# Kernel tuning notes

Measured on AMD Instinct MI355X. Metric: run time of the kernel, lower is better.

Reference implementation:

```python
import jax, jax.numpy as jnp
import numpy as np

B, T, C = 2, 2048, 1024
H, HD = 16, 64
M = 256  # per memory bank
K_CANON = 4


def setup_inputs() -> dict:
    key = jax.random.key(0)
    ks = jax.random.split(key, 10)
    s = 0.02
    return {
        "x": jax.random.normal(ks[0], (B, T, C), jnp.float32),
        "fwd_mem": jax.random.normal(ks[1], (B, M, C), jnp.float32),
        "rev_mem": jax.random.normal(ks[2], (B, M, C), jnp.float32),
        "Wq": jax.random.normal(ks[3], (C, C), jnp.float32) * s,
        "Wk": jax.random.normal(ks[4], (C, C), jnp.float32) * s,
        "Wv": jax.random.normal(ks[5], (C, C), jnp.float32) * s,
        "Wo": jax.random.normal(ks[6], (C, C), jnp.float32) * s,
        "gate_w": jax.random.normal(ks[7], (H, C), jnp.float32) * s,
        "gate_b": jnp.zeros((H,), jnp.float32),
        "canon_w": jax.random.normal(ks[8], (C, 1, K_CANON), jnp.float32) * s,
        "canon_bias": jax.random.normal(ks[9], (C,), jnp.float32) * s,
    }


def _canon_conv(y, canon_w, canon_bias):
    # causal depthwise conv1d with residual; torch weight [C,1,K] -> WIO kernel [K,1,C]
    kern = jnp.transpose(canon_w, (2, 1, 0))
    y_pad = jnp.pad(y, ((0, 0), (K_CANON - 1, 0), (0, 0)))
    conv = jax.lax.conv_general_dilated(
        y_pad, kern, window_strides=(1,), padding='VALID',
        dimension_numbers=('NWC', 'WIO', 'NWC'), feature_group_count=C)
    return y + conv + canon_bias


def reference(x, fwd_mem, rev_mem, Wq, Wk, Wv, Wo, gate_w, gate_b, canon_w, canon_bias):
    Bn, Tn, Cn = x.shape
    scale = 1.0 / np.sqrt(HD)

    q = x @ Wq.T  # [B,T,C]
    k = x @ Wk.T
    v = x @ Wv.T
    # memory integration: project memories with same k/v proj, concat on seq dim
    k = jnp.concatenate([k, fwd_mem @ Wk.T, rev_mem @ Wk.T], axis=1)  # [B,S,C]
    v = jnp.concatenate([v, fwd_mem @ Wv.T, rev_mem @ Wv.T], axis=1)
    S = k.shape[1]
    mem_len = S - Tn

    def heads(t):
        return t.reshape(Bn, -1, H, HD).transpose(0, 2, 1, 3)  # [B,h,S,hd]

    qh, kh, vh = heads(q), heads(k), heads(v)
    scores = jnp.einsum('bhtd,bhsd->bhts', qh, kh) * scale  # [B,h,T,S]
    # causal mask over the first T key columns; memory columns fully visible
    causal = jnp.triu(jnp.ones((Tn, Tn), bool), k=1)
    full_mask = jnp.pad(causal, ((0, 0), (0, mem_len)))  # [T,S]
    scores = jnp.where(full_mask[None, None], -jnp.inf, scores)
    w = jax.nn.softmax(scores, axis=-1)

    # split chunk vs memory, gate memory contribution per head
    w_chunk, w_mem = w[..., :Tn], w[..., Tn:]
    v_chunk, v_mem = vh[:, :, :Tn], vh[:, :, Tn:]
    Y_chunk = jnp.einsum('bhts,bhsd->bhtd', w_chunk, v_chunk)
    Y_mem = jnp.einsum('bhtm,bhmd->bhtd', w_mem, v_mem)
    g = jax.nn.sigmoid(q @ gate_w.T + gate_b)  # [B,T,h]
    g = g.transpose(0, 2, 1)[..., None]  # [B,h,T,1]
    Y = Y_chunk + g * Y_mem

    attn_out = Y.transpose(0, 2, 1, 3).reshape(Bn, Tn, Cn)
    attn_out = _canon_conv(attn_out, canon_w, canon_bias)
    return attn_out @ Wo.T
```

## Files before the change

kernel.cpp:

```cpp
#include <hip/hip_runtime.h>
#include <hip/hip_bf16.h>
#include <cstdint>


typedef __bf16 bf16x8_t __attribute__((ext_vector_type(8)));
typedef __bf16 bf16x4_t __attribute__((ext_vector_type(4)));
typedef float f32x4_t __attribute__((ext_vector_type(4)));

__device__ __forceinline__ f32x4_t mfma16(bf16x8_t a, bf16x8_t b, f32x4_t c) {
    return __builtin_amdgcn_mfma_f32_16x16x32_bf16(a, b, c, 0, 0, 0);
}

__device__ __forceinline__ void gl2lds16(const void* g, void* l) {
    __builtin_amdgcn_global_load_lds(
        (__attribute__((address_space(1))) uint32_t*)(uintptr_t)g,
        (__attribute__((address_space(3))) uint32_t*)l, 16, 0, 0);
}

#define OFF_X   0
#define OFF_FWD 4194304
#define OFF_REV 4718592
#define OFF_WQ  5242880
#define OFF_WK  6291456
#define OFF_WV  7340032
#define OFF_WO  8388608
#define OFF_GW  9437184
#define OFF_GB  9453568
#define OFF_CW  9453584
#define OFF_CB  9457680
#define N_TOT   9458704

__global__ __launch_bounds__(256) void conv_all_kernel(
    const void* p0, const void* p1, const void* p2, const void* p3,
    const void* p4, const void* p5, const void* p6, const void* p7,
    const void* p8, const void* p9, const void* p10,
    __hip_bfloat16* __restrict__ arena)
{
    const int i = (blockIdx.x * 256 + threadIdx.x) * 4;
    if (i >= N_TOT) return;
    const void* src; int off;
    if      (i < OFF_FWD) { src = p0;  off = OFF_X;   }
    else if (i < OFF_REV) { src = p1;  off = OFF_FWD; }
    else if (i < OFF_WQ)  { src = p2;  off = OFF_REV; }
    else if (i < OFF_WK)  { src = p3;  off = OFF_WQ;  }
    else if (i < OFF_WV)  { src = p4;  off = OFF_WK;  }
    else if (i < OFF_WO)  { src = p5;  off = OFF_WV;  }
    else if (i < OFF_GW)  { src = p6;  off = OFF_WO;  }
    else if (i < OFF_GB)  { src = p7;  off = OFF_GW;  }
    else if (i < OFF_CW)  { src = p8;  off = OFF_GB;  }
    else if (i < OFF_CB)  { src = p9;  off = OFF_CW;  }
    else                  { src = p10; off = OFF_CB;  }
    const int j = i - off;
    const float4 f = *(const float4*)((const float*)src + j);
    arena[i + 0] = __float2bfloat16(f.x);
    arena[i + 1] = __float2bfloat16(f.y);
    arena[i + 2] = __float2bfloat16(f.z);
    arena[i + 3] = __float2bfloat16(f.w);
}

__device__ __forceinline__ void gemm_core(
    const __hip_bfloat16* __restrict__ A, const __hip_bfloat16* __restrict__ B,
    void* __restrict__ C, int ldc, int f32o, int arow0, int brow0,
    __hip_bfloat16* As, __hip_bfloat16* Bs)
{
    const int tid  = threadIdx.x;
    const int lane = tid & 63;
    const int wid  = tid >> 6;
    const int q4   = lane >> 4;
    const int c16  = lane & 15;
    const int wm   = (wid >> 1) * 64;
    const int wn   = (wid & 1) * 64;
    const int c0 = tid;
    const int c1 = tid + 256;
    const __hip_bfloat16* gA0 = A + (size_t)(arow0 + (c0 >> 2)) * 1024 + ((c0 & 3) << 3);
    const __hip_bfloat16* gA1 = A + (size_t)(arow0 + (c1 >> 2)) * 1024 + ((c1 & 3) << 3);
    const __hip_bfloat16* gB0 = B + (size_t)(brow0 + (c0 >> 2)) * 1024 + ((c0 & 3) << 3);
    const __hip_bfloat16* gB1 = B + (size_t)(brow0 + (c1 >> 2)) * 1024 + ((c1 & 3) << 3);

    f32x4_t acc[4][4];
#pragma unroll
    for (int i = 0; i < 4; ++i)
#pragma unroll
        for (int j = 0; j < 4; ++j)
#pragma unroll
            for (int r = 0; r < 4; ++r) acc[i][j][r] = 0.0f;

    gl2lds16(gA0, As + c0 * 8);
    gl2lds16(gA1, As + c1 * 8);
    gl2lds16(gB0, Bs + c0 * 8);
    gl2lds16(gB1, Bs + c1 * 8);

    for (int it = 0; it < 32; ++it) {
        __hip_bfloat16* curA = As + (it & 1) * 4096;
        __hip_bfloat16* curB = Bs + (it & 1) * 4096;
        __syncthreads();
        if (it < 31) {
            const int nk = (it + 1) * 32;
            __hip_bfloat16* nA = As + ((it + 1) & 1) * 4096;
            __hip_bfloat16* nB = Bs + ((it + 1) & 1) * 4096;
            gl2lds16(gA0 + nk, nA + c0 * 8);
            gl2lds16(gA1 + nk, nA + c1 * 8);
            gl2lds16(gB0 + nk, nB + c0 * 8);
            gl2lds16(gB1 + nk, nB + c1 * 8);
        }
        bf16x8_t af[4], bfr[4];
#pragma unroll
        for (int i = 0; i < 4; ++i)
            af[i] = *(const bf16x8_t*)&curA[(wm + i * 16 + c16) * 32 + q4 * 8];
#pragma unroll
        for (int j = 0; j < 4; ++j)
            bfr[j] = *(const bf16x8_t*)&curB[(wn + j * 16 + c16) * 32 + q4 * 8];
#pragma unroll
        for (int i = 0; i < 4; ++i)
#pragma unroll
            for (int j = 0; j < 4; ++j)
                acc[i][j] = mfma16(af[i], bfr[j], acc[i][j]);
    }
#pragma unroll
    for (int i = 0; i < 4; ++i) {
        const int mg = arow0 + wm + i * 16 + q4 * 4;
#pragma unroll
        for (int j = 0; j < 4; ++j) {
            const int ng = brow0 + wn + j * 16 + c16;
#pragma unroll
            for (int r = 0; r < 4; ++r) {
                const size_t idx = (size_t)(mg + r) * ldc + ng;
                if (f32o) ((float*)C)[idx] = acc[i][j][r];
                else ((__hip_bfloat16*)C)[idx] = __float2bfloat16(acc[i][j][r]);
            }
        }
    }
}

__global__ __launch_bounds__(256) void qkv_kernel(
    const __hip_bfloat16* __restrict__ x, const __hip_bfloat16* __restrict__ Wqk,
    const __hip_bfloat16* __restrict__ Wv,
    __hip_bfloat16* __restrict__ QK, __hip_bfloat16* __restrict__ Vt)
{
    __shared__ __align__(16) __hip_bfloat16 As[2 * 128 * 32];
    __shared__ __align__(16) __hip_bfloat16 Bs[2 * 128 * 32];
    int id = blockIdx.x;
    if (id < 640)
        gemm_core(x, Wqk, QK, 2048, 0, (id >> 4) * 128, (id & 15) * 128, As, Bs);
    else {
        id -= 640;
        gemm_core(Wv, x, Vt, 5120, 0, (id & 7) * 128, (id >> 3) * 128, As, Bs);
    }
}

__global__ __launch_bounds__(256) void gemm_bt_kernel(
    const __hip_bfloat16* __restrict__ A, const __hip_bfloat16* __restrict__ B,
    void* __restrict__ C, int ldc, int f32o)
{
    __shared__ __align__(16) __hip_bfloat16 As[2 * 128 * 32];
    __shared__ __align__(16) __hip_bfloat16 Bs[2 * 128 * 32];
    gemm_core(A, B, C, ldc, f32o, blockIdx.x * 128, blockIdx.y * 128, As, Bs);
}

__global__ __launch_bounds__(64) void gate_kernel(
    const __hip_bfloat16* __restrict__ QK, const __hip_bfloat16* __restrict__ gw,
    const __hip_bfloat16* __restrict__ gb, float* __restrict__ G)
{
    const int base = blockIdx.x * 16;
    const int lane = threadIdx.x;
    const int q4   = lane >> 4;
    const int c16  = lane & 15;
    f32x4_t acc = {0.0f, 0.0f, 0.0f, 0.0f};
    const __hip_bfloat16* qrow = QK + (size_t)(base + c16) * 2048 + q4 * 8;
    const __hip_bfloat16* wrow = gw + (size_t)c16 * 1024 + q4 * 8;
#pragma unroll
    for (int kk = 0; kk < 32; ++kk) {
        const bf16x8_t a = *(const bf16x8_t*)(qrow + kk * 32);
        const bf16x8_t w = *(const bf16x8_t*)(wrow + kk * 32);
        acc = mfma16(a, w, acc);
    }
    const float bias = __bfloat162float(gb[c16]);
#pragma unroll
    for (int r = 0; r < 4; ++r) {
        const int row = base + q4 * 4 + r;
        G[(size_t)row * 16 + c16] = 1.0f / (1.0f + __expf(-(acc[r] + bias)));
    }
}

#define PSTR 72
__global__ __launch_bounds__(256) void attn_kernel(
    const __hip_bfloat16* __restrict__ QK,
    const __hip_bfloat16* __restrict__ Vt,
    const float* __restrict__ G, __hip_bfloat16* __restrict__ Y)
{
    __shared__ __align__(16) __hip_bfloat16 Ks[64 * 64];
    __shared__ __align__(16) __hip_bfloat16 Vs[64 * 64];
    __shared__ __align__(16) __hip_bfloat16 Plds[4][16 * PSTR];
    const int flat = blockIdx.x;
    const int bh   = flat & 31;
    const int tIdx = 31 - (flat >> 5);
    const int b    = bh >> 4;
    const int h    = bh & 15;
    const int tid  = threadIdx.x;
    const int wid  = tid >> 6;
    const int lane = tid & 63;
    const int q4   = lane >> 4;
    const int c16  = lane & 15;
    const int rowbase = tIdx * 64 + wid * 16;

    const __hip_bfloat16* qrow = QK + (size_t)(b * 2048 + rowbase + c16) * 2048 + h * 64;
    const bf16x8_t qa0 = *(const bf16x8_t*)(qrow + q4 * 8);
    const bf16x8_t qa1 = *(const bf16x8_t*)(qrow + 32 + q4 * 8);

    float rs[4], gate[4];
    f32x4_t acc[4];
#pragma unroll
    for (int fp = 0; fp < 4; ++fp)
#pragma unroll
        for (int r = 0; r < 4; ++r) acc[fp][r] = 0.0f;
#pragma unroll
    for (int r = 0; r < 4; ++r) {
        rs[r] = 0.0f;
        gate[r] = G[(size_t)(b * 2048 + rowbase + q4 * 4 + r) * 16 + h];
    }

    const int nCausal = tIdx + 1;
    const int nTiles  = nCausal + 8;
    auto kvRow = [&](int tile) -> int {
        if (tile < nCausal) return b * 2048 + tile * 64;
        const int mi = (tile - nCausal) * 64;
        return (mi < 256) ? 4096 + b * 256 + mi : 4608 + b * 256 + (mi - 256);
    };

    const int srow0 = tid >> 3,         sch0 = (tid & 7) ^ (srow0 & 7);
    const int srow1 = (tid + 256) >> 3, sch1 = (tid & 7) ^ (srow1 & 7);
    const int sw0 = (q4 ^ (c16 & 7)) * 8;
    const int sw1 = ((q4 + 4) ^ (c16 & 7)) * 8;
    const __hip_bfloat16* Kbase = QK + 1024 + h * 64;

    for (int tile = 0; tile < nTiles; ++tile) {
        const bool isMem  = (tile >= nCausal);
        const bool isDiag = (tile == nCausal - 1);
        const int  vr     = kvRow(tile);
        __syncthreads();
        gl2lds16(Kbase + (size_t)(vr + srow0) * 2048 + sch0 * 8, &Ks[tid * 8]);
        gl2lds16(Kbase + (size_t)(vr + srow1) * 2048 + sch1 * 8, &Ks[(tid + 256) * 8]);
        gl2lds16(Vt + (size_t)(h * 64 + srow0) * 5120 + vr + sch0 * 8, &Vs[tid * 8]);
        gl2lds16(Vt + (size_t)(h * 64 + srow1) * 5120 + vr + sch1 * 8, &Vs[(tid + 256) * 8]);
        __syncthreads();
        bf16x8_t kb0[4], kb1[4], vb0[4], vb1[4];
#pragma unroll
        for (int f = 0; f < 4; ++f) {
            kb0[f] = *(const bf16x8_t*)&Ks[(f * 16 + c16) * 64 + sw0];
            kb1[f] = *(const bf16x8_t*)&Ks[(f * 16 + c16) * 64 + sw1];
            vb0[f] = *(const bf16x8_t*)&Vs[(f * 16 + c16) * 64 + sw0];
            vb1[f] = *(const bf16x8_t*)&Vs[(f * 16 + c16) * 64 + sw1];
        }
        f32x4_t sc[4];
#pragma unroll
        for (int f = 0; f < 4; ++f) {
            f32x4_t z = {0.0f, 0.0f, 0.0f, 0.0f};
            z = mfma16(qa0, kb0[f], z);
            z = mfma16(qa1, kb1[f], z);
            sc[f] = z;
        }
#pragma unroll
        for (int f = 0; f < 4; ++f)
#pragma unroll
            for (int r = 0; r < 4; ++r) {
                float p = __expf(sc[f][r] * 0.125f);
                if (isDiag) {
                    const int sg = tile * 64 + f * 16 + c16;
                    if (sg > rowbase + q4 * 4 + r) p = 0.0f;
                }
                rs[r] += p;
                if (isMem) p *= gate[r];
                Plds[wid][(q4 * 4 + r) * PSTR + f * 16 + c16] = __float2bfloat16(p);
            }
        const bf16x8_t pa0 = *(const bf16x8_t*)&Plds[wid][c16 * PSTR + q4 * 8];
        const bf16x8_t pa1 = *(const bf16x8_t*)&Plds[wid][c16 * PSTR + 32 + q4 * 8];
#pragma unroll
        for (int fp = 0; fp < 4; ++fp) {
            acc[fp] = mfma16(pa0, vb0[fp], acc[fp]);
            acc[fp] = mfma16(pa1, vb1[fp], acc[fp]);
        }
    }
#pragma unroll
    for (int m = 1; m <= 8; m <<= 1)
#pragma unroll
        for (int r = 0; r < 4; ++r) rs[r] += __shfl_xor(rs[r], m, 64);
    float inv[4];
#pragma unroll
    for (int r = 0; r < 4; ++r) inv[r] = 1.0f / rs[r];
#pragma unroll
    for (int fp = 0; fp < 4; ++fp)
#pragma unroll
        for (int r = 0; r < 4; ++r) {
            const int tg = rowbase + q4 * 4 + r;
            Y[(size_t)(b * 2048 + tg) * 1024 + h * 64 + fp * 16 + c16] =
                __float2bfloat16(acc[fp][r] * inv[r]);
        }
}

__global__ __launch_bounds__(256) void canon_kernel(
    const __hip_bfloat16* __restrict__ Yin, const __hip_bfloat16* __restrict__ cw,
    const __hip_bfloat16* __restrict__ cb, __hip_bfloat16* __restrict__ Yout)
{
    const int idx = (blockIdx.x * 256 + threadIdx.x) * 4;
    const int c = idx & 1023;
    const int t = (idx >> 10) & 2047;
    const bf16x4_t y0 = *(const bf16x4_t*)(Yin + idx);
    const bf16x4_t bb = *(const bf16x4_t*)(cb + c);
    float a[4];
#pragma unroll
    for (int i = 0; i < 4; ++i) a[i] = (float)y0[i] + (float)bb[i];
    const bf16x8_t w01 = *(const bf16x8_t*)(cw + c * 4);
    const bf16x8_t w23 = *(const bf16x8_t*)(cw + c * 4 + 8);
#pragma unroll
    for (int j = 0; j < 4; ++j) {
        if (t - 3 + j >= 0) {
            const bf16x4_t yj = *(const bf16x4_t*)(Yin + idx + (j - 3) * 1024);
            a[0] += (float)yj[0] * (float)w01[j];
            a[1] += (float)yj[1] * (float)w01[4 + j];
            a[2] += (float)yj[2] * (float)w23[j];
            a[3] += (float)yj[3] * (float)w23[4 + j];
        }
    }
    bf16x4_t o;
#pragma unroll
    for (int i = 0; i < 4; ++i) o[i] = (__bf16)a[i];
    *(bf16x4_t*)(Yout + idx) = o;
}

extern "C" void kernel_launch(void* const* d_in, const int* in_sizes, int n_in,
                              void* d_out, int out_size, void* d_ws, size_t ws_size,
                              hipStream_t stream)
{
    char* ws = (char*)d_ws;
    const size_t MB = 1ull << 20;
    if (ws_size < 50 * MB) return;

    __hip_bfloat16* arena = (__hip_bfloat16*)ws;
    __hip_bfloat16* QK    = (__hip_bfloat16*)(ws + 19 * MB);
    __hip_bfloat16* Vt    = (__hip_bfloat16*)(ws + 39 * MB);
    float*          G     = (float*)(ws + 49 * MB);
    __hip_bfloat16* Y1    = (__hip_bfloat16*)ws;
    __hip_bfloat16* Y2    = QK;

    const dim3 blk(256);
    conv_all_kernel<<<dim3((N_TOT / 4 + 255) / 256), blk, 0, stream>>>(
        d_in[0], d_in[1], d_in[2], d_in[3], d_in[4], d_in[5], d_in[6],
        d_in[7], d_in[8], d_in[9], d_in[10], arena);

    const __hip_bfloat16* xB  = arena + OFF_X;
    const __hip_bfloat16* WqB = arena + OFF_WQ;
    const __hip_bfloat16* WvB = arena + OFF_WV;
    const __hip_bfloat16* WoB = arena + OFF_WO;

    qkv_kernel<<<dim3(960), blk, 0, stream>>>(xB, WqB, WvB, QK, Vt);
    gate_kernel<<<dim3(256), dim3(64), 0, stream>>>(QK, arena + OFF_GW, arena + OFF_GB, G);
    attn_kernel<<<dim3(1024), blk, 0, stream>>>(QK, Vt, G, Y1);
    canon_kernel<<<dim3(4096), blk, 0, stream>>>(Y1, arena + OFF_CW, arena + OFF_CB, Y2);
    gemm_bt_kernel<<<dim3(32, 8), blk, 0, stream>>>(Y2, WoB, d_out, 1024, 1);
}
```

Baseline: 241.2 us.

## Double-buffer K/V tiles in attention and compute row sums with MFMA

The attention kernel now keeps two LDS buffers for K and V. It prefetches the next tile while computing the current one, which removes one barrier per tile and hides global load latency behind MFMA work. Row sums of the probabilities come from an MFMA against a ones vector instead of scalar adds and shuffles. Chunk and memory contributions go into separate accumulators, and the gate is applied once in the epilogue rather than per element. The softmax uses exp2 with the log2(e) factor folded into the scale. The costs are doubled K/V LDS usage, which may lower occupancy, extra accumulator registers, and row sums now taken from bf16-rounded probabilities.

After: 248.7 us. 3.1% more time.

```diff
diff --git a/kernel.cpp b/kernel.cpp
--- a/kernel.cpp
+++ b/kernel.cpp
@@ -188,8 +188,8 @@
     const __hip_bfloat16* __restrict__ Vt,
     const float* __restrict__ G, __hip_bfloat16* __restrict__ Y)
 {
-    __shared__ __align__(16) __hip_bfloat16 Ks[64 * 64];
-    __shared__ __align__(16) __hip_bfloat16 Vs[64 * 64];
+    __shared__ __align__(16) __hip_bfloat16 Ks[2][64 * 64];
+    __shared__ __align__(16) __hip_bfloat16 Vs[2][64 * 64];
     __shared__ __align__(16) __hip_bfloat16 Plds[4][16 * PSTR];
     const int flat = blockIdx.x;
     const int bh   = flat & 31;
@@ -207,17 +207,17 @@
     const bf16x8_t qa0 = *(const bf16x8_t*)(qrow + q4 * 8);
     const bf16x8_t qa1 = *(const bf16x8_t*)(qrow + 32 + q4 * 8);
 
-    float rs[4], gate[4];
-    f32x4_t acc[4];
+    bf16x8_t ones;
+#pragma unroll
+    for (int i = 0; i < 8; ++i) ones[i] = (__bf16)1.0f;
+
+    f32x4_t accC[4], accM[4];
+    f32x4_t rsC = {0.0f, 0.0f, 0.0f, 0.0f};
+    f32x4_t rsM = {0.0f, 0.0f, 0.0f, 0.0f};
 #pragma unroll
     for (int fp = 0; fp < 4; ++fp)
 #pragma unroll
-        for (int r = 0; r < 4; ++r) acc[fp][r] = 0.0f;
-#pragma unroll
-    for (int r = 0; r < 4; ++r) {
-        rs[r] = 0.0f;
-        gate[r] = G[(size_t)(b * 2048 + rowbase + q4 * 4 + r) * 16 + h];
-    }
+        for (int r = 0; r < 4; ++r) { accC[fp][r] = 0.0f; accM[fp][r] = 0.0f; }
 
     const int nCausal = tIdx + 1;
     const int nTiles  = nCausal + 8;
@@ -233,23 +233,36 @@
     const int sw1 = ((q4 + 4) ^ (c16 & 7)) * 8;
     const __hip_bfloat16* Kbase = QK + 1024 + h * 64;
 
+    {
+        const int vr0 = kvRow(0);
+        gl2lds16(Kbase + (size_t)(vr0 + srow0) * 2048 + sch0 * 8, &Ks[0][tid * 8]);
+        gl2lds16(Kbase + (size_t)(vr0 + srow1) * 2048 + sch1 * 8, &Ks[0][(tid + 256) * 8]);
+        gl2lds16(Vt + (size_t)(h * 64 + srow0) * 5120 + vr0 + sch0 * 8, &Vs[0][tid * 8]);
+        gl2lds16(Vt + (size_t)(h * 64 + srow1) * 5120 + vr0 + sch1 * 8, &Vs[0][(tid + 256) * 8]);
+    }
+
+    const float SCL = 0.18033688f;
+
     for (int tile = 0; tile < nTiles; ++tile) {
+        const int cur = tile & 1;
+        __syncthreads();
+        if (tile + 1 < nTiles) {
+            const int nxt = cur ^ 1;
+            const int vr  = kvRow(tile + 1);
+            gl2lds16(Kbase + (size_t)(vr + srow0) * 2048 + sch0 * 8, &Ks[nxt][tid * 8]);
+            gl2lds16(Kbase + (size_t)(vr + srow1) * 2048 + sch1 * 8, &Ks[nxt][(tid + 256) * 8]);
+            gl2lds16(Vt + (size_t)(h * 64 + srow0) * 5120 + vr + sch0 * 8, &Vs[nxt][tid * 8]);
+            gl2lds16(Vt + (size_t)(h * 64 + srow1) * 5120 + vr + sch1 * 8, &Vs[nxt][(tid + 256) * 8]);
+        }
         const bool isMem  = (tile >= nCausal);
         const bool isDiag = (tile == nCausal - 1);
-        const int  vr     = kvRow(tile);
-        __syncthreads();
-        gl2lds16(Kbase + (size_t)(vr + srow0) * 2048 + sch0 * 8, &Ks[tid * 8]);
-        gl2lds16(Kbase + (size_t)(vr + srow1) * 2048 + sch1 * 8, &Ks[(tid + 256) * 8]);
-        gl2lds16(Vt + (size_t)(h * 64 + srow0) * 5120 + vr + sch0 * 8, &Vs[tid * 8]);
-        gl2lds16(Vt + (size_t)(h * 64 + srow1) * 5120 + vr + sch1 * 8, &Vs[(tid + 256) * 8]);
-        __syncthreads();
         bf16x8_t kb0[4], kb1[4], vb0[4], vb1[4];
 #pragma unroll
         for (int f = 0; f < 4; ++f) {
-            kb0[f] = *(const bf16x8_t*)&Ks[(f * 16 + c16) * 64 + sw0];
-            kb1[f] = *(const bf16x8_t*)&Ks[(f * 16 + c16) * 64 + sw1];
-            vb0[f] = *(const bf16x8_t*)&Vs[(f * 16 + c16) * 64 + sw0];
-            vb1[f] = *(const bf16x8_t*)&Vs[(f * 16 + c16) * 64 + sw1];
+            kb0[f] = *(const bf16x8_t*)&Ks[cur][(f * 16 + c16) * 64 + sw0];
+            kb1[f] = *(const bf16x8_t*)&Ks[cur][(f * 16 + c16) * 64 + sw1];
+            vb0[f] = *(const bf16x8_t*)&Vs[cur][(f * 16 + c16) * 64 + sw0];
+            vb1[f] = *(const bf16x8_t*)&Vs[cur][(f * 16 + c16) * 64 + sw1];
         }
         f32x4_t sc[4];
 #pragma unroll
@@ -263,37 +276,47 @@
         for (int f = 0; f < 4; ++f)
 #pragma unroll
             for (int r = 0; r < 4; ++r) {
-                float p = __expf(sc[f][r] * 0.125f);
+                float p = __builtin_amdgcn_exp2f(sc[f][r] * SCL);
                 if (isDiag) {
-                    const int sg = tile * 64 + f * 16 + c16;
-                    if (sg > rowbase + q4 * 4 + r) p = 0.0f;
+                    const int sg = f * 16 + c16;
+                    if (sg > wid * 16 + q4 * 4 + r) p = 0.0f;
                 }
-                rs[r] += p;
-                if (isMem) p *= gate[r];
                 Plds[wid][(q4 * 4 + r) * PSTR + f * 16 + c16] = __float2bfloat16(p);
             }
         const bf16x8_t pa0 = *(const bf16x8_t*)&Plds[wid][c16 * PSTR + q4 * 8];
         const bf16x8_t pa1 = *(const bf16x8_t*)&Plds[wid][c16 * PSTR + 32 + q4 * 8];
-#pragma unroll
-        for (int fp = 0; fp < 4; ++fp) {
-            acc[fp] = mfma16(pa0, vb0[fp], acc[fp]);
-            acc[fp] = mfma16(pa1, vb1[fp], acc[fp]);
-        }
-    }
-#pragma unroll
-    for (int m = 1; m <= 8; m <<= 1)
-#pragma unroll
-        for (int r = 0; r < 4; ++r) rs[r] += __shfl_xor(rs[r], m, 64);
-    float inv[4];
-#pragma unroll
-    for (int r = 0; r < 4; ++r) inv[r] = 1.0f / rs[r];
+        if (isMem) {
+            rsM = mfma16(pa0, ones, rsM);
+            rsM = mfma16(pa1, ones, rsM);
+#pragma unroll
+            for (int fp = 0; fp < 4; ++fp) {
+                accM[fp] = mfma16(pa0, vb0[fp], accM[fp]);
+                accM[fp] = mfma16(pa1, vb1[fp], accM[fp]);
+            }
+        } else {
+            rsC = mfma16(pa0, ones, rsC);
+            rsC = mfma16(pa1, ones, rsC);
+#pragma unroll
+            for (int fp = 0; fp < 4; ++fp) {
+                accC[fp] = mfma16(pa0, vb0[fp], accC[fp]);
+                accC[fp] = mfma16(pa1, vb1[fp], accC[fp]);
+            }
+        }
+    }
+
+    float inv[4], gate[4];
+#pragma unroll
+    for (int r = 0; r < 4; ++r) {
+        gate[r] = G[(size_t)(b * 2048 + rowbase + q4 * 4 + r) * 16 + h];
+        inv[r] = 1.0f / (rsC[r] + rsM[r]);
+    }
 #pragma unroll
     for (int fp = 0; fp < 4; ++fp)
 #pragma unroll
         for (int r = 0; r < 4; ++r) {
             const int tg = rowbase + q4 * 4 + r;
             Y[(size_t)(b * 2048 + tg) * 1024 + h * 64 + fp * 16 + c16] =
-                __float2bfloat16(acc[fp][r] * inv[r]);
+                __float2bfloat16((accC[fp][r] + gate[r] * accM[fp][r]) * inv[r]);
         }
 }
 
```

## Load K/V fragments directly from global memory, drop LDS staging and block barriers

Applied to the files above, without the earlier changes.

The attention kernel no longer stages each K/V tile into shared memory with barriers. Each wave now reads its K and V MFMA fragments straight from global memory, relying on L1/L2 to serve the reuse across the four waves. The P scratch buffer switches from a padded stride to an XOR-swizzled layout, exp is computed via exp2 with a prescaled constant, the diagonal mask compare is simplified, and launch bounds request 4 blocks per SM. This removes the two __syncthreads per tile and frees LDS for occupancy, at the cost of redundant global/cache traffic per wave and less-coalesced strided loads.

After: 380.0 us. 57.5% more time.

```diff
diff --git a/kernel.cpp b/kernel.cpp
--- a/kernel.cpp
+++ b/kernel.cpp
@@ -182,15 +182,12 @@
     }
 }
 
-#define PSTR 72
-__global__ __launch_bounds__(256) void attn_kernel(
+__global__ __launch_bounds__(256, 4) void attn_kernel(
     const __hip_bfloat16* __restrict__ QK,
     const __hip_bfloat16* __restrict__ Vt,
     const float* __restrict__ G, __hip_bfloat16* __restrict__ Y)
 {
-    __shared__ __align__(16) __hip_bfloat16 Ks[64 * 64];
-    __shared__ __align__(16) __hip_bfloat16 Vs[64 * 64];
-    __shared__ __align__(16) __hip_bfloat16 Plds[4][16 * PSTR];
+    __shared__ __align__(16) __hip_bfloat16 Plds[4][16 * 64];
     const int flat = blockIdx.x;
     const int bh   = flat & 31;
     const int tIdx = 31 - (flat >> 5);
@@ -227,29 +224,24 @@
         return (mi < 256) ? 4096 + b * 256 + mi : 4608 + b * 256 + (mi - 256);
     };
 
-    const int srow0 = tid >> 3,         sch0 = (tid & 7) ^ (srow0 & 7);
-    const int srow1 = (tid + 256) >> 3, sch1 = (tid & 7) ^ (srow1 & 7);
-    const int sw0 = (q4 ^ (c16 & 7)) * 8;
-    const int sw1 = ((q4 + 4) ^ (c16 & 7)) * 8;
-    const __hip_bfloat16* Kbase = QK + 1024 + h * 64;
+    const __hip_bfloat16* Kfb = QK + 1024 + (size_t)h * 64 + (size_t)c16 * 2048 + q4 * 8;
+    const __hip_bfloat16* Vfb = Vt + (size_t)(h * 64 + c16) * 5120 + q4 * 8;
+
+    const float SCL = 0.18033688f;
 
     for (int tile = 0; tile < nTiles; ++tile) {
         const bool isMem  = (tile >= nCausal);
         const bool isDiag = (tile == nCausal - 1);
         const int  vr     = kvRow(tile);
-        __syncthreads();
-        gl2lds16(Kbase + (size_t)(vr + srow0) * 2048 + sch0 * 8, &Ks[tid * 8]);
-        gl2lds16(Kbase + (size_t)(vr + srow1) * 2048 + sch1 * 8, &Ks[(tid + 256) * 8]);
-        gl2lds16(Vt + (size_t)(h * 64 + srow0) * 5120 + vr + sch0 * 8, &Vs[tid * 8]);
-        gl2lds16(Vt + (size_t)(h * 64 + srow1) * 5120 + vr + sch1 * 8, &Vs[(tid + 256) * 8]);
-        __syncthreads();
+        const __hip_bfloat16* kp = Kfb + (size_t)vr * 2048;
+        const __hip_bfloat16* vp = Vfb + vr;
         bf16x8_t kb0[4], kb1[4], vb0[4], vb1[4];
 #pragma unroll
         for (int f = 0; f < 4; ++f) {
-            kb0[f] = *(const bf16x8_t*)&Ks[(f * 16 + c16) * 64 + sw0];
-            kb1[f] = *(const bf16x8_t*)&Ks[(f * 16 + c16) * 64 + sw1];
-            vb0[f] = *(const bf16x8_t*)&Vs[(f * 16 + c16) * 64 + sw0];
-            vb1[f] = *(const bf16x8_t*)&Vs[(f * 16 + c16) * 64 + sw1];
+            kb0[f] = *(const bf16x8_t*)(kp + (size_t)f * 16 * 2048);
+            kb1[f] = *(const bf16x8_t*)(kp + (size_t)f * 16 * 2048 + 32);
+            vb0[f] = *(const bf16x8_t*)(vp + (size_t)f * 16 * 5120);
+            vb1[f] = *(const bf16x8_t*)(vp + (size_t)f * 16 * 5120 + 32);
         }
         f32x4_t sc[4];
 #pragma unroll
@@ -263,17 +255,22 @@
         for (int f = 0; f < 4; ++f)
 #pragma unroll
             for (int r = 0; r < 4; ++r) {
-                float p = __expf(sc[f][r] * 0.125f);
+                float p = __builtin_amdgcn_exp2f(sc[f][r] * SCL);
                 if (isDiag) {
-                    const int sg = tile * 64 + f * 16 + c16;
-                    if (sg > rowbase + q4 * 4 + r) p = 0.0f;
+                    const int sg = f * 16 + c16;
+                    if (sg > wid * 16 + q4 * 4 + r) p = 0.0f;
                 }
                 rs[r] += p;
                 if (isMem) p *= gate[r];
-                Plds[wid][(q4 * 4 + r) * PSTR + f * 16 + c16] = __float2bfloat16(p);
+                const int prow = q4 * 4 + r;
+                const int pcol = f * 16 + c16;
+                Plds[wid][prow * 64 + (((pcol >> 3) ^ (prow & 7)) << 3) + (pcol & 7)] =
+                    __float2bfloat16(p);
             }
-        const bf16x8_t pa0 = *(const bf16x8_t*)&Plds[wid][c16 * PSTR + q4 * 8];
-        const bf16x8_t pa1 = *(const bf16x8_t*)&Plds[wid][c16 * PSTR + 32 + q4 * 8];
+        const int sw0 = (q4 ^ (c16 & 7)) * 8;
+        const int sw1 = ((q4 + 4) ^ (c16 & 7)) * 8;
+        const bf16x8_t pa0 = *(const bf16x8_t*)&Plds[wid][c16 * 64 + sw0];
+        const bf16x8_t pa1 = *(const bf16x8_t*)&Plds[wid][c16 * 64 + sw1];
 #pragma unroll
         for (int fp = 0; fp < 4; ++fp) {
             acc[fp] = mfma16(pa0, vb0[fp], acc[fp]);
```
